# Kernel tuning notes

Measured on AMD Instinct MI355X. Metric: run time of the kernel, lower is better.

## Reference

```python
import jax, jax.numpy as jnp
import numpy as np

N_NODES = 100000
N_EDGES = 600000
N_GRAPHS = 8
D_IN = 256
H = 128
N_CONV = 2  # layers [128,128,128] -> first_h + 2 GINConvs
BN_EPS = 1e-5


def _bn_eval(x, p):
    # p: [4, H] rows = (gamma, beta, running_mean, running_var); eval-mode BatchNorm1d
    g, b, m, v = p[0], p[1], p[2], p[3]
    return (x - m) * jax.lax.rsqrt(v + BN_EPS) * g + b


def setup_inputs() -> dict:
    key = jax.random.key(0)
    ks = jax.random.split(key, 12)
    x = jax.random.normal(ks[0], (N_NODES, D_IN), dtype=jnp.float32)
    edge_index = jax.random.randint(ks[1], (2, N_EDGES), 0, N_NODES, dtype=jnp.int64 if jax.config.jax_enable_x64 else jnp.int32)
    batch = jnp.sort(jax.random.randint(ks[2], (N_NODES,), 0, N_GRAPHS))
    s = 0.05
    w_first = jax.random.normal(ks[3], (D_IN, H), dtype=jnp.float32) * s
    b_first = jax.random.normal(ks[4], (H,), dtype=jnp.float32) * s

    def bn_params(k):
        k1, k2, k3, k4 = jax.random.split(k, 4)
        gamma = jax.random.uniform(k1, (H,), minval=0.5, maxval=1.5)
        beta = jax.random.normal(k2, (H,)) * 0.1
        mean = jax.random.normal(k3, (H,)) * 0.1
        var = jax.random.uniform(k4, (H,), minval=0.5, maxval=1.5)
        return jnp.stack([gamma, beta, mean, var])  # [4, H]

    bn_first = bn_params(ks[5])
    w_conv = jax.random.normal(ks[6], (N_CONV, H, H), dtype=jnp.float32) * s
    b_conv = jax.random.normal(ks[7], (N_CONV, H), dtype=jnp.float32) * s
    bn_conv = jnp.stack([bn_params(k) for k in jax.random.split(ks[8], N_CONV)])  # [2,4,H]
    w_lin = jax.random.normal(ks[9], (N_CONV + 1, H, 1), dtype=jnp.float32) * s
    b_lin = jax.random.normal(ks[10], (N_CONV + 1, 1), dtype=jnp.float32) * s
    return {"x": x, "edge_index": edge_index, "batch": batch,
            "w_first": w_first, "b_first": b_first, "bn_first": bn_first,
            "w_conv": w_conv, "b_conv": b_conv, "bn_conv": bn_conv,
            "w_lin": w_lin, "b_lin": b_lin}


def reference(x, edge_index, batch, w_first, b_first, bn_first, w_conv, b_conv, bn_conv, w_lin, b_lin):
    src, dst = edge_index[0], edge_index[1]
    # first_h: Linear + BN(eval) + ReLU
    h = jax.nn.relu(_bn_eval(x @ w_first + b_first, bn_first))  # [N, H]

    # layer 0: node-level linear head + global max pool
    node_pred = h @ w_lin[0] + b_lin[0]  # [N, 1]
    wsi_pred = jax.ops.segment_max(node_pred, batch, num_segments=N_GRAPHS)  # [G, 1]

    for l in range(N_CONV):
        # GINConv (eps=0, sum aggregation): nn((1+eps)*x_i + sum_{j->i} x_j)
        agg = jax.ops.segment_sum(h[src], dst, num_segments=N_NODES)  # [N, H]
        h = jax.nn.relu(_bn_eval((h + agg) @ w_conv[l] + b_conv[l], bn_conv[l]))
        np_sub = h @ w_lin[l + 1] + b_lin[l + 1]  # [N, 1]
        node_pred = node_pred + np_sub
        wsi_pred = wsi_pred + jax.ops.segment_max(np_sub, batch, num_segments=N_GRAPHS)
        # dropout p=0.0 -> identity
    return wsi_pred, node_pred
```

## Files before the change

### kernel.cpp

```cpp
#include <hip/hip_runtime.h>
#include <hip/hip_bf16.h>

#define H 128
#define D_IN 256
#define NGRAPH 8

typedef __attribute__((ext_vector_type(8))) short bf16x8;
typedef __attribute__((ext_vector_type(4))) float f32x4;
typedef __attribute__((ext_vector_type(4))) int i32x4;

__device__ __forceinline__ unsigned fenc(float f) {
  unsigned u = __float_as_uint(f);
  return (u & 0x80000000u) ? ~u : (u | 0x80000000u);
}
__device__ __forceinline__ float fdec(unsigned e) {
  unsigned v = (e & 0x80000000u) ? (e & 0x7FFFFFFFu) : ~e;
  return __uint_as_float(v);
}
__device__ __forceinline__ unsigned short f2bf(float f) {
  unsigned u = __float_as_uint(f);
  unsigned r = u + 0x7FFFu + ((u >> 16) & 1u);
  return (unsigned short)(r >> 16);
}

__device__ __forceinline__ void gload16(const void* gsrc, void* ldst) {
  __builtin_amdgcn_global_load_lds(
      (const __attribute__((address_space(1))) unsigned int*)gsrc,
      (__attribute__((address_space(3))) unsigned int*)ldst, 16, 0, 0);
}

__global__ void init_kernel(int* __restrict__ offsets, int n1) {
  int i = blockIdx.x * blockDim.x + threadIdx.x;
  if (i < n1) offsets[i] = 0;
}

__global__ void count_kernel(const int* __restrict__ dst, int* __restrict__ offsets, int E) {
  int i = blockIdx.x * blockDim.x + threadIdx.x;
  int stride = gridDim.x * blockDim.x;
  for (int e = i; e < E; e += stride) atomicAdd(&offsets[dst[e]], 1);
}

__global__ void __launch_bounds__(1024)
scan_local(int* __restrict__ data, int* __restrict__ bsum, int n) {
  __shared__ int s[1024];
  int tid = threadIdx.x;
  int i = blockIdx.x * 1024 + tid;
  int v = (i < n) ? data[i] : 0;
  s[tid] = v;
  __syncthreads();
  for (int off = 1; off < 1024; off <<= 1) {
    int t = (tid >= off) ? s[tid - off] : 0;
    __syncthreads();
    s[tid] += t;
    __syncthreads();
  }
  if (i < n) data[i] = s[tid] - v;
  if (tid == 1023) bsum[blockIdx.x] = s[1023];
}

__global__ void __launch_bounds__(128)
scan_bsum(int* __restrict__ bsum, int nb) {
  __shared__ int s[128];
  int tid = threadIdx.x;
  int v = (tid < nb) ? bsum[tid] : 0;
  s[tid] = v;
  __syncthreads();
  for (int off = 1; off < 128; off <<= 1) {
    int t = (tid >= off) ? s[tid - off] : 0;
    __syncthreads();
    s[tid] += t;
    __syncthreads();
  }
  if (tid < nb) bsum[tid] = s[tid] - v;
}

__global__ void __launch_bounds__(1024)
scan_add(int* __restrict__ data, const int* __restrict__ bsum, int* __restrict__ cursor,
         int n, int ncur) {
  int i = blockIdx.x * 1024 + threadIdx.x;
  if (i < n) {
    int v = data[i] + bsum[blockIdx.x];
    data[i] = v;
    if (i < ncur) cursor[i] = v;
  }
}

__global__ void fill_kernel(const int* __restrict__ src, const int* __restrict__ dst,
                            int* __restrict__ cursor, int* __restrict__ esrc, int E) {
  int i = blockIdx.x * blockDim.x + threadIdx.x;
  int stride = gridDim.x * blockDim.x;
  for (int e = i; e < E; e += stride) {
    int d = dst[e];
    int p = atomicAdd(&cursor[d], 1);
    esrc[p] = src[e];
  }
}

__global__ void prep_weights(const float* __restrict__ wf, const float* __restrict__ wcv,
                             unsigned short* __restrict__ Bf, unsigned short* __restrict__ Bc) {
  int i = blockIdx.x * 256 + threadIdx.x;
  if (i < 32768) {
    int s = i >> 12, r = i & 4095;
    int c = r >> 5, r2 = r & 31;
    int g = r2 >> 3, j = r2 & 7;
    int k = s * 32 + g * 8 + j;
    Bf[i] = f2bf(wf[k * H + c]);
  } else {
    int i2 = i - 32768;
    int l = i2 >> 14, r = i2 & 16383;
    int s = r >> 12, rr = r & 4095;
    int c = rr >> 5, r2 = rr & 31;
    int g = r2 >> 3, j = r2 & 7;
    int k = s * 32 + g * 8 + j;
    Bc[i2] = f2bf(wcv[l * H * H + k * H + c]);
  }
}

template <int K, bool AF32, bool FIRST>
__global__ void __launch_bounds__(256, 4)
gemm_kernel(const void* __restrict__ Ain, const unsigned short* __restrict__ Bpack,
            const float* __restrict__ bias, const float* __restrict__ bn,
            const float* __restrict__ wlin, const float* __restrict__ blin, int lidx,
            const int* __restrict__ batch, unsigned short* __restrict__ hout,
            float* __restrict__ node_pred, unsigned* __restrict__ slot, int N) {
  constexpr int RB = 256;
  constexpr int ROWBYTES = AF32 ? K * 4 : K * 2;
  constexpr int NCHUNK = ROWBYTES / RB;
  constexpr int SPC = AF32 ? 2 : 4;
  __shared__ char s_a[64 * RB];
  __shared__ float s_head[64][2];
  __shared__ unsigned s_wsi[NGRAPH];
  const int tid = threadIdx.x;
  const int wid = tid >> 6, lane = tid & 63;
  const int wr = wid >> 1, wc = wid & 1;
  const int g = lane >> 4, l15 = lane & 15;
  const int row0blk = blockIdx.x * 64;
  if (tid < NGRAPH) s_wsi[tid] = 0u;

  f32x4 acc[2][4] = {};
  const int lrow0 = wr * 32;
  const char* Ab = (const char*)Ain;

  for (int ch = 0; ch < NCHUNK; ++ch) {
#pragma unroll
    for (int it = 0; it < 4; ++it) {
      int unit = it * 256 + tid;
      int lr = unit >> 4;
      int cb = (unit & 15) * 16;
      int grow = row0blk + lr;
      grow = (grow < N) ? grow : (N - 1);
      int gcol = cb ^ ((lr & 7) << 4);
      gload16(Ab + (size_t)grow * ROWBYTES + ch * RB + gcol,
              s_a + (it * 256 + wid * 64) * 16);
    }
    __syncthreads();

#pragma unroll
    for (int s = 0; s < SPC; ++s) {
      int sg = ch * SPC + s;
      bf16x8 bfr[4];
#pragma unroll
      for (int n = 0; n < 4; ++n) {
        int c = wc * 64 + n * 16 + l15;
        bfr[n] = *(const bf16x8*)(Bpack + sg * 4096 + c * 32 + g * 8);
      }
      bf16x8 af[2];
#pragma unroll
      for (int m = 0; m < 2; ++m) {
        int lr = lrow0 + m * 16 + l15;
        int sw = (lr & 7) << 4;
        if (AF32) {
          int c0 = s * 128 + g * 32;
          f32x4 u0 = *(const f32x4*)(s_a + lr * RB + (c0 ^ sw));
          f32x4 u1 = *(const f32x4*)(s_a + lr * RB + ((c0 + 16) ^ sw));
          union { unsigned short hh[8]; bf16x8 v; } pk;
          pk.hh[0] = f2bf(u0[0]); pk.hh[1] = f2bf(u0[1]);
          pk.hh[2] = f2bf(u0[2]); pk.hh[3] = f2bf(u0[3]);
          pk.hh[4] = f2bf(u1[0]); pk.hh[5] = f2bf(u1[1]);
          pk.hh[6] = f2bf(u1[2]); pk.hh[7] = f2bf(u1[3]);
          af[m] = pk.v;
        } else {
          int c0 = s * 64 + g * 16;
          af[m] = *(const bf16x8*)(s_a + lr * RB + (c0 ^ sw));
        }
      }
#pragma unroll
      for (int m = 0; m < 2; ++m)
#pragma unroll
        for (int n = 0; n < 4; ++n)
          acc[m][n] = __builtin_amdgcn_mfma_f32_16x16x32_bf16(af[m], bfr[n], acc[m][n], 0, 0, 0);
    }
    __syncthreads();
  }

  float sc[4], sh[4], wl[4];
#pragma unroll
  for (int n = 0; n < 4; ++n) {
    int c = wc * 64 + n * 16 + l15;
    float gam = bn[c], bet = bn[H + c], mu = bn[2 * H + c], va = bn[3 * H + c];
    float rs = rsqrtf(va + 1e-5f);
    sc[n] = gam * rs;
    sh[n] = (bias[c] - mu) * gam * rs + bet;
    wl[n] = wlin[c];
  }

  char* aw = s_a + wid * 2048;
#pragma unroll
  for (int m = 0; m < 2; ++m) {
    float pj[4] = {0.f, 0.f, 0.f, 0.f};
#pragma unroll
    for (int n = 0; n < 4; ++n)
#pragma unroll
      for (int j = 0; j < 4; ++j) {
        float hv = fmaxf(acc[m][n][j] * sc[n] + sh[n], 0.f);
        pj[j] += hv * wl[n];
        *(unsigned short*)(aw + (g * 4 + j) * 128 + (n * 16 + l15) * 2) = f2bf(hv);
      }
#pragma unroll
    for (int j = 0; j < 4; ++j) {
      pj[j] += __shfl_xor(pj[j], 1);
      pj[j] += __shfl_xor(pj[j], 2);
      pj[j] += __shfl_xor(pj[j], 4);
      pj[j] += __shfl_xor(pj[j], 8);
    }
    if (l15 == 0) {
#pragma unroll
      for (int j = 0; j < 4; ++j)
        s_head[wr * 32 + m * 16 + g * 4 + j][wc] = pj[j];
    }
    int grb = row0blk + wr * 32 + m * 16;
#pragma unroll
    for (int it = 0; it < 2; ++it) {
      int bo = lane * 16 + it * 1024;
      int r16 = bo >> 7, inrow = bo & 127;
      if (grb + r16 < N)
        *(i32x4*)((char*)hout + (size_t)(grb + r16) * 256 + wc * 128 + inrow) =
            *(i32x4*)(aw + bo);
    }
  }
  __syncthreads();
  if (tid < 64) {
    int grh = row0blk + tid;
    if (grh < N) {
      float np = s_head[tid][0] + s_head[tid][1] + blin[lidx];
      if (FIRST) node_pred[grh] = np; else node_pred[grh] += np;
      atomicMax(&s_wsi[batch[grh]], fenc(np));
    }
  }
  __syncthreads();
  if (tid < NGRAPH) slot[blockIdx.x * NGRAPH + tid] = s_wsi[tid];
}

__global__ void __launch_bounds__(256)
agg_kernel(const unsigned short* __restrict__ h, const int* __restrict__ offsets,
           const int* __restrict__ esrc, unsigned short* __restrict__ tmp, int n) {
  int node = blockIdx.x * 4 + (threadIdx.x >> 6);
  if (node >= n) return;
  int lane = threadIdx.x & 63;
  const unsigned* hw = (const unsigned*)h;
  size_t base = (size_t)node * (H / 2) + lane;
  unsigned u = hw[base];
  float a0 = __uint_as_float((u & 0xFFFFu) << 16);
  float a1 = __uint_as_float(u & 0xFFFF0000u);
  int s = offsets[node], e = offsets[node + 1];
  int j = s;
  for (; j + 4 <= e; j += 4) {
    int i0 = esrc[j], i1 = esrc[j + 1], i2 = esrc[j + 2], i3 = esrc[j + 3];
    unsigned v0 = hw[(size_t)i0 * (H / 2) + lane];
    unsigned v1 = hw[(size_t)i1 * (H / 2) + lane];
    unsigned v2 = hw[(size_t)i2 * (H / 2) + lane];
    unsigned v3 = hw[(size_t)i3 * (H / 2) + lane];
    a0 += __uint_as_float((v0 & 0xFFFFu) << 16) + __uint_as_float((v1 & 0xFFFFu) << 16) +
          __uint_as_float((v2 & 0xFFFFu) << 16) + __uint_as_float((v3 & 0xFFFFu) << 16);
    a1 += __uint_as_float(v0 & 0xFFFF0000u) + __uint_as_float(v1 & 0xFFFF0000u) +
          __uint_as_float(v2 & 0xFFFF0000u) + __uint_as_float(v3 & 0xFFFF0000u);
  }
  for (; j < e; ++j) {
    unsigned v2 = hw[(size_t)esrc[j] * (H / 2) + lane];
    a0 += __uint_as_float((v2 & 0xFFFFu) << 16);
    a1 += __uint_as_float(v2 & 0xFFFF0000u);
  }
  unsigned r = ((unsigned)f2bf(a1) << 16) | (unsigned)f2bf(a0);
  ((unsigned*)tmp)[base] = r;
}

__global__ void __launch_bounds__(256)
finalize_kernel(const unsigned* __restrict__ slots, float* __restrict__ out, int nb) {
  __shared__ float red[3][NGRAPH];
  int tid = threadIdx.x;
  if (tid < 192) {
    int pair = tid >> 3, w = tid & 7;
    int l = pair >> 3, g = pair & 7;
    unsigned m = 0u;
    const unsigned* base = slots + (size_t)l * nb * NGRAPH + g;
    for (int b = w; b < nb; b += 8) m = max(m, base[b * NGRAPH]);
    m = max(m, (unsigned)__shfl_xor((int)m, 1));
    m = max(m, (unsigned)__shfl_xor((int)m, 2));
    m = max(m, (unsigned)__shfl_xor((int)m, 4));
    if (w == 0) red[l][g] = fdec(m);
  }
  __syncthreads();
  if (tid < NGRAPH) out[tid] = red[0][tid] + red[1][tid] + red[2][tid];
}

extern "C" void kernel_launch(void* const* d_in, const int* in_sizes, int n_in,
                              void* d_out, int out_size, void* d_ws, size_t ws_size,
                              hipStream_t stream) {
  const float* x        = (const float*)d_in[0];
  const int*   ei       = (const int*)d_in[1];
  const int*   batch    = (const int*)d_in[2];
  const float* w_first  = (const float*)d_in[3];
  const float* b_first  = (const float*)d_in[4];
  const float* bn_first = (const float*)d_in[5];
  const float* w_conv   = (const float*)d_in[6];
  const float* b_conv   = (const float*)d_in[7];
  const float* bn_conv  = (const float*)d_in[8];
  const float* w_lin    = (const float*)d_in[9];
  const float* b_lin    = (const float*)d_in[10];
  float* out = (float*)d_out;

  const int N = in_sizes[0] / D_IN;
  const int E = in_sizes[1] / 2;
  const int* src = ei;
  const int* dst = ei + E;

  const int gemm_grid = (N + 63) / 64;

  char* ws = (char*)d_ws;
  unsigned short* h   = (unsigned short*)ws;
  unsigned short* tmp = h + (size_t)N * H;
  unsigned short* wTf = tmp + (size_t)N * H;
  unsigned short* wTc = wTf + H * D_IN;
  int* offsets = (int*)(wTc + 2 * H * H);
  int* cursor  = offsets + (N + 1);
  int* esrc    = cursor + N;
  int* bsum    = esrc + E;
  unsigned* slots = (unsigned*)(bsum + 128);
  float* node_pred = out + NGRAPH;

  const int nscan = N + 1;
  const int nb = (nscan + 1023) / 1024;

  init_kernel<<<(N + 256) / 256, 256, 0, stream>>>(offsets, N + 1);
  count_kernel<<<1024, 256, 0, stream>>>(dst, offsets, E);
  scan_local<<<nb, 1024, 0, stream>>>(offsets, bsum, nscan);
  scan_bsum<<<1, 128, 0, stream>>>(bsum, nb);
  scan_add<<<nb, 1024, 0, stream>>>(offsets, bsum, cursor, nscan, N);
  fill_kernel<<<1024, 256, 0, stream>>>(src, dst, cursor, esrc, E);
  prep_weights<<<256, 256, 0, stream>>>(w_first, w_conv, wTf, wTc);

  gemm_kernel<D_IN, true, true><<<gemm_grid, 256, 0, stream>>>(
      x, wTf, b_first, bn_first, w_lin, b_lin, 0, batch, h, node_pred, slots, N);
  for (int l = 0; l < 2; ++l) {
    agg_kernel<<<(N + 3) / 4, 256, 0, stream>>>(h, offsets, esrc, tmp, N);
    gemm_kernel<H, false, false><<<gemm_grid, 256, 0, stream>>>(
        tmp, wTc + (size_t)l * 16384, b_conv + (size_t)l * H, bn_conv + (size_t)l * 4 * H,
        w_lin + (size_t)(l + 1) * H, b_lin, l + 1, batch, h, node_pred,
        slots + (size_t)(l + 1) * gemm_grid * NGRAPH, N);
  }
  finalize_kernel<<<1, 256, 0, stream>>>(slots, out, gemm_grid);
}
```

Before: 253.1 us.

## Fuse whole pipeline into one cooperative persistent kernel with grid syncs

Replaces the chain of about a dozen kernel launches with a single cooperative mega-kernel, capped at 768 blocks, that uses grid.sync between the CSR build, weight packing, GEMM and aggregation phases. Per-block max-pool slots and the finalize reduction are replaced by global atomicMax into a small per-layer array. The aim is to remove launch gaps and inter-kernel drain overhead. In exchange, GEMM and aggregation now run persistent loops over tiles at lower occupancy, and each grid barrier has its own cost. A multi-kernel fallback path is kept in case the cooperative launch fails.

```diff
diff --git a/kernel.cpp b/kernel.cpp
--- a/kernel.cpp
+++ b/kernel.cpp
@@ -1,5 +1,8 @@
 #include <hip/hip_runtime.h>
 #include <hip/hip_bf16.h>
+#include <hip/hip_cooperative_groups.h>
+
+namespace cg = cooperative_groups;
 
 #define H 128
 #define D_IN 256
@@ -22,119 +25,30 @@
   unsigned r = u + 0x7FFFu + ((u >> 16) & 1u);
   return (unsigned short)(r >> 16);
 }
-
 __device__ __forceinline__ void gload16(const void* gsrc, void* ldst) {
   __builtin_amdgcn_global_load_lds(
       (const __attribute__((address_space(1))) unsigned int*)gsrc,
       (__attribute__((address_space(3))) unsigned int*)ldst, 16, 0, 0);
 }
 
-__global__ void init_kernel(int* __restrict__ offsets, int n1) {
-  int i = blockIdx.x * blockDim.x + threadIdx.x;
-  if (i < n1) offsets[i] = 0;
-}
-
-__global__ void count_kernel(const int* __restrict__ dst, int* __restrict__ offsets, int E) {
-  int i = blockIdx.x * blockDim.x + threadIdx.x;
-  int stride = gridDim.x * blockDim.x;
-  for (int e = i; e < E; e += stride) atomicAdd(&offsets[dst[e]], 1);
-}
-
-__global__ void __launch_bounds__(1024)
-scan_local(int* __restrict__ data, int* __restrict__ bsum, int n) {
-  __shared__ int s[1024];
-  int tid = threadIdx.x;
-  int i = blockIdx.x * 1024 + tid;
-  int v = (i < n) ? data[i] : 0;
-  s[tid] = v;
-  __syncthreads();
-  for (int off = 1; off < 1024; off <<= 1) {
-    int t = (tid >= off) ? s[tid - off] : 0;
-    __syncthreads();
-    s[tid] += t;
-    __syncthreads();
-  }
-  if (i < n) data[i] = s[tid] - v;
-  if (tid == 1023) bsum[blockIdx.x] = s[1023];
-}
-
-__global__ void __launch_bounds__(128)
-scan_bsum(int* __restrict__ bsum, int nb) {
-  __shared__ int s[128];
-  int tid = threadIdx.x;
-  int v = (tid < nb) ? bsum[tid] : 0;
-  s[tid] = v;
-  __syncthreads();
-  for (int off = 1; off < 128; off <<= 1) {
-    int t = (tid >= off) ? s[tid - off] : 0;
-    __syncthreads();
-    s[tid] += t;
-    __syncthreads();
-  }
-  if (tid < nb) bsum[tid] = s[tid] - v;
-}
-
-__global__ void __launch_bounds__(1024)
-scan_add(int* __restrict__ data, const int* __restrict__ bsum, int* __restrict__ cursor,
-         int n, int ncur) {
-  int i = blockIdx.x * 1024 + threadIdx.x;
-  if (i < n) {
-    int v = data[i] + bsum[blockIdx.x];
-    data[i] = v;
-    if (i < ncur) cursor[i] = v;
-  }
-}
-
-__global__ void fill_kernel(const int* __restrict__ src, const int* __restrict__ dst,
-                            int* __restrict__ cursor, int* __restrict__ esrc, int E) {
-  int i = blockIdx.x * blockDim.x + threadIdx.x;
-  int stride = gridDim.x * blockDim.x;
-  for (int e = i; e < E; e += stride) {
-    int d = dst[e];
-    int p = atomicAdd(&cursor[d], 1);
-    esrc[p] = src[e];
-  }
-}
-
-__global__ void prep_weights(const float* __restrict__ wf, const float* __restrict__ wcv,
-                             unsigned short* __restrict__ Bf, unsigned short* __restrict__ Bc) {
-  int i = blockIdx.x * 256 + threadIdx.x;
-  if (i < 32768) {
-    int s = i >> 12, r = i & 4095;
-    int c = r >> 5, r2 = r & 31;
-    int g = r2 >> 3, j = r2 & 7;
-    int k = s * 32 + g * 8 + j;
-    Bf[i] = f2bf(wf[k * H + c]);
-  } else {
-    int i2 = i - 32768;
-    int l = i2 >> 14, r = i2 & 16383;
-    int s = r >> 12, rr = r & 4095;
-    int c = rr >> 5, r2 = rr & 31;
-    int g = r2 >> 3, j = r2 & 7;
-    int k = s * 32 + g * 8 + j;
-    Bc[i2] = f2bf(wcv[l * H * H + k * H + c]);
-  }
-}
 
 template <int K, bool AF32, bool FIRST>
-__global__ void __launch_bounds__(256, 4)
-gemm_kernel(const void* __restrict__ Ain, const unsigned short* __restrict__ Bpack,
-            const float* __restrict__ bias, const float* __restrict__ bn,
-            const float* __restrict__ wlin, const float* __restrict__ blin, int lidx,
-            const int* __restrict__ batch, unsigned short* __restrict__ hout,
-            float* __restrict__ node_pred, unsigned* __restrict__ slot, int N) {
+__device__ void gemm_tile(int tile, const void* Ain, const unsigned short* Bpack,
+                          const float* bias, const float* bn, const float* wlin,
+                          float blinv, const int* batch, unsigned short* hout,
+                          float* node_pred, unsigned* wsiL, int N,
+                          char* s_a, float (*s_head)[2], unsigned* s_wsi) {
   constexpr int RB = 256;
   constexpr int ROWBYTES = AF32 ? K * 4 : K * 2;
   constexpr int NCHUNK = ROWBYTES / RB;
   constexpr int SPC = AF32 ? 2 : 4;
-  __shared__ char s_a[64 * RB];
-  __shared__ float s_head[64][2];
-  __shared__ unsigned s_wsi[NGRAPH];
   const int tid = threadIdx.x;
   const int wid = tid >> 6, lane = tid & 63;
   const int wr = wid >> 1, wc = wid & 1;
   const int g = lane >> 4, l15 = lane & 15;
-  const int row0blk = blockIdx.x * 64;
+  const int row0blk = tile * 64;
+
+  __syncthreads();
   if (tid < NGRAPH) s_wsi[tid] = 0u;
 
   f32x4 acc[2][4] = {};
@@ -242,121 +156,364 @@
   if (tid < 64) {
     int grh = row0blk + tid;
     if (grh < N) {
-      float np = s_head[tid][0] + s_head[tid][1] + blin[lidx];
+      float np = s_head[tid][0] + s_head[tid][1] + blinv;
       if (FIRST) node_pred[grh] = np; else node_pred[grh] += np;
       atomicMax(&s_wsi[batch[grh]], fenc(np));
     }
   }
   __syncthreads();
-  if (tid < NGRAPH) slot[blockIdx.x * NGRAPH + tid] = s_wsi[tid];
+  if (tid < NGRAPH && s_wsi[tid] != 0u) atomicMax(&wsiL[tid], s_wsi[tid]);
+}
+
+__device__ void agg_body(const unsigned short* h, const int* offsets, const int* esrc,
+                         unsigned short* tmp, int N) {
+  const int tid = threadIdx.x;
+  const int wid = tid >> 6, lane = tid & 63;
+  const int stride = gridDim.x * 4;
+  const unsigned* hw = (const unsigned*)h;
+  for (int node = blockIdx.x * 4 + wid; node < N; node += stride) {
+    size_t base = (size_t)node * 64 + lane;
+    unsigned u = hw[base];
+    float a0 = __uint_as_float((u & 0xFFFFu) << 16);
+    float a1 = __uint_as_float(u & 0xFFFF0000u);
+    int s = offsets[node], e = offsets[node + 1];
+    int j = s;
+    for (; j + 4 <= e; j += 4) {
+      int i0 = esrc[j], i1 = esrc[j + 1], i2 = esrc[j + 2], i3 = esrc[j + 3];
+      unsigned v0 = hw[(size_t)i0 * 64 + lane];
+      unsigned v1 = hw[(size_t)i1 * 64 + lane];
+      unsigned v2 = hw[(size_t)i2 * 64 + lane];
+      unsigned v3 = hw[(size_t)i3 * 64 + lane];
+      a0 += __uint_as_float((v0 & 0xFFFFu) << 16) + __uint_as_float((v1 & 0xFFFFu) << 16) +
+            __uint_as_float((v2 & 0xFFFFu) << 16) + __uint_as_float((v3 & 0xFFFFu) << 16);
+      a1 += __uint_as_float(v0 & 0xFFFF0000u) + __uint_as_float(v1 & 0xFFFF0000u) +
+            __uint_as_float(v2 & 0xFFFF0000u) + __uint_as_float(v3 & 0xFFFF0000u);
+    }
+    for (; j < e; ++j) {
+      unsigned v = hw[(size_t)esrc[j] * 64 + lane];
+      a0 += __uint_as_float((v & 0xFFFFu) << 16);
+      a1 += __uint_as_float(v & 0xFFFF0000u);
+    }
+    ((unsigned*)tmp)[base] = ((unsigned)f2bf(a1) << 16) | (unsigned)f2bf(a0);
+  }
+}
+
+__device__ void pack_weights_body(int i, const float* wf, const float* wcv,
+                                  unsigned short* Bf, unsigned short* Bc) {
+  if (i < 32768) {
+    int s = i >> 12, r = i & 4095;
+    int c = r >> 5, r2 = r & 31;
+    int g = r2 >> 3, j = r2 & 7;
+    int k = s * 32 + g * 8 + j;
+    Bf[i] = f2bf(wf[k * H + c]);
+  } else if (i < 65536) {
+    int i2 = i - 32768;
+    int l = i2 >> 14, r = i2 & 16383;
+    int s = r >> 12, rr = r & 4095;
+    int c = rr >> 5, r2 = rr & 31;
+    int g = r2 >> 3, j = r2 & 7;
+    int k = s * 32 + g * 8 + j;
+    Bc[i2] = f2bf(wcv[l * H * H + k * H + c]);
+  }
+}
+
+
+struct KArgs {
+  const float* x;
+  const int* src;
+  const int* dst;
+  const int* batch;
+  const float* w_first;
+  const float* b_first;
+  const float* bn_first;
+  const float* w_conv;
+  const float* b_conv;
+  const float* bn_conv;
+  const float* w_lin;
+  const float* b_lin;
+  float* out;
+  unsigned short* h;
+  unsigned short* tmp;
+  unsigned short* wTf;
+  unsigned short* wTc;
+  int* offsets;
+  int* cursor;
+  int* esrc;
+  int* csum;
+  unsigned* wsi;
+  int N, E, ntiles, nchunks;
+};
+
+__global__ void __launch_bounds__(256)
+mega_kernel(KArgs a) {
+  cg::grid_group grid = cg::this_grid();
+  __shared__ char s_a[16384];
+  __shared__ float s_head[64][2];
+  __shared__ unsigned s_wsi[NGRAPH];
+  int* s_scan = (int*)s_a;
+  int* s_c2 = (int*)(s_a + 1024);
+
+  const int tid = threadIdx.x;
+  const int bid = blockIdx.x;
+  const int gtid = bid * 256 + tid;
+  const int gstride = gridDim.x * 256;
+  const int n1 = a.N + 1;
+
+  for (int i = gtid; i < n1; i += gstride) a.offsets[i] = 0;
+  if (gtid < 3 * NGRAPH) a.wsi[gtid] = 0u;
+  for (int i = gtid; i < 65536; i += gstride)
+    pack_weights_body(i, a.w_first, a.w_conv, a.wTf, a.wTc);
+  grid.sync();
+
+  for (int e = gtid; e < a.E; e += gstride) atomicAdd(&a.offsets[a.dst[e]], 1);
+  grid.sync();
+
+  for (int ch = bid; ch < a.nchunks; ch += gridDim.x) {
+    int i = ch * 256 + tid;
+    int v = (i < n1) ? a.offsets[i] : 0;
+    s_scan[tid] = v;
+    __syncthreads();
+    for (int off = 1; off < 256; off <<= 1) {
+      int t = (tid >= off) ? s_scan[tid - off] : 0;
+      __syncthreads();
+      s_scan[tid] += t;
+      __syncthreads();
+    }
+    if (i < n1) a.offsets[i] = s_scan[tid] - v;
+    if (tid == 255) a.csum[ch] = s_scan[255];
+    __syncthreads();
+  }
+  grid.sync();
+
+  if (bid == 0) {
+    for (int k = tid; k < 512; k += 256) s_c2[k] = (k < a.nchunks) ? a.csum[k] : 0;
+    __syncthreads();
+    for (int off = 1; off < 512; off <<= 1) {
+      int t0 = (tid >= off) ? s_c2[tid - off] : 0;
+      int t1 = ((tid + 256) >= off) ? s_c2[tid + 256 - off] : 0;
+      __syncthreads();
+      s_c2[tid] += t0;
+      s_c2[tid + 256] += t1;
+      __syncthreads();
+    }
+    for (int k = tid; k < a.nchunks; k += 256) a.csum[k] = (k == 0) ? 0 : s_c2[k - 1];
+  }
+  grid.sync();
+
+  for (int i = gtid; i < n1; i += gstride) {
+    int v = a.offsets[i] + a.csum[i >> 8];
+    a.offsets[i] = v;
+    if (i < a.N) a.cursor[i] = v;
+  }
+  grid.sync();
+
+  for (int e = gtid; e < a.E; e += gstride) {
+    int d = a.dst[e];
+    int p = atomicAdd(&a.cursor[d], 1);
+    a.esrc[p] = a.src[e];
+  }
+  grid.sync();
+
+  float* node_pred = a.out + NGRAPH;
+
+  for (int t = bid; t < a.ntiles; t += gridDim.x)
+    gemm_tile<D_IN, true, true>(t, a.x, a.wTf, a.b_first, a.bn_first, a.w_lin,
+                                a.b_lin[0], a.batch, a.h, node_pred, a.wsi, a.N,
+                                s_a, s_head, s_wsi);
+  grid.sync();
+
+  agg_body(a.h, a.offsets, a.esrc, a.tmp, a.N);
+  grid.sync();
+
+  for (int t = bid; t < a.ntiles; t += gridDim.x)
+    gemm_tile<H, false, false>(t, a.tmp, a.wTc, a.b_conv, a.bn_conv, a.w_lin + H,
+                               a.b_lin[1], a.batch, a.h, node_pred, a.wsi + NGRAPH, a.N,
+                               s_a, s_head, s_wsi);
+  grid.sync();
+
+  agg_body(a.h, a.offsets, a.esrc, a.tmp, a.N);
+  grid.sync();
+
+  for (int t = bid; t < a.ntiles; t += gridDim.x)
+    gemm_tile<H, false, false>(t, a.tmp, a.wTc + 16384, a.b_conv + H, a.bn_conv + 4 * H,
+                               a.w_lin + 2 * H, a.b_lin[2], a.batch, a.h, node_pred,
+                               a.wsi + 2 * NGRAPH, a.N, s_a, s_head, s_wsi);
+  grid.sync();
+
+  if (bid == 0 && tid < NGRAPH)
+    a.out[tid] = fdec(a.wsi[tid]) + fdec(a.wsi[NGRAPH + tid]) + fdec(a.wsi[2 * NGRAPH + tid]);
+}
+
+
+__global__ void init_prep_kernel(int* __restrict__ offsets, int n1, unsigned* __restrict__ wsi,
+                                 const float* __restrict__ wf, const float* __restrict__ wcv,
+                                 unsigned short* __restrict__ Bf, unsigned short* __restrict__ Bc) {
+  int i = blockIdx.x * 256 + threadIdx.x;
+  if (i < n1) offsets[i] = 0;
+  if (i < 3 * NGRAPH) wsi[i] = 0u;
+  pack_weights_body(i, wf, wcv, Bf, Bc);
+}
+
+__global__ void count_kernel(const int* __restrict__ dst, int* __restrict__ offsets, int E) {
+  int i = blockIdx.x * blockDim.x + threadIdx.x;
+  int stride = gridDim.x * blockDim.x;
+  for (int e = i; e < E; e += stride) atomicAdd(&offsets[dst[e]], 1);
+}
+
+__global__ void __launch_bounds__(1024)
+scan_local(int* __restrict__ data, int* __restrict__ bsum, int n) {
+  __shared__ int s[1024];
+  int tid = threadIdx.x;
+  int i = blockIdx.x * 1024 + tid;
+  int v = (i < n) ? data[i] : 0;
+  s[tid] = v;
+  __syncthreads();
+  for (int off = 1; off < 1024; off <<= 1) {
+    int t = (tid >= off) ? s[tid - off] : 0;
+    __syncthreads();
+    s[tid] += t;
+    __syncthreads();
+  }
+  if (i < n) data[i] = s[tid] - v;
+  if (tid == 1023) bsum[blockIdx.x] = s[1023];
+}
+
+__global__ void __launch_bounds__(1024)
+scan_add2(int* __restrict__ data, const int* __restrict__ bsum, int* __restrict__ cursor,
+          int n, int ncur, int nb) {
+  __shared__ int sb[128];
+  int tid = threadIdx.x;
+  if (tid < 128) sb[tid] = (tid < nb) ? bsum[tid] : 0;
+  __syncthreads();
+  for (int off = 1; off < 128; off <<= 1) {
+    int t = (tid < 128 && tid >= off) ? sb[tid - off] : 0;
+    __syncthreads();
+    if (tid < 128) sb[tid] += t;
+    __syncthreads();
+  }
+  int add = (blockIdx.x == 0) ? 0 : sb[blockIdx.x - 1];
+  int i = blockIdx.x * 1024 + tid;
+  if (i < n) {
+    int v = data[i] + add;
+    data[i] = v;
+    if (i < ncur) cursor[i] = v;
+  }
+}
+
+__global__ void fill_kernel(const int* __restrict__ src, const int* __restrict__ dst,
+                            int* __restrict__ cursor, int* __restrict__ esrc, int E) {
+  int i = blockIdx.x * blockDim.x + threadIdx.x;
+  int stride = gridDim.x * blockDim.x;
+  for (int e = i; e < E; e += stride) {
+    int d = dst[e];
+    int p = atomicAdd(&cursor[d], 1);
+    esrc[p] = src[e];
+  }
+}
+
+template <int K, bool AF32, bool FIRST>
+__global__ void __launch_bounds__(256, 4)
+gemm_kernel(const void* __restrict__ Ain, const unsigned short* __restrict__ Bpack,
+            const float* __restrict__ bias, const float* __restrict__ bn,
+            const float* __restrict__ wlin, const float* __restrict__ blin, int lidx,
+            const int* __restrict__ batch, unsigned short* __restrict__ hout,
+            float* __restrict__ node_pred, unsigned* __restrict__ wsi, int N) {
+  __shared__ char s_a[16384];
+  __shared__ float s_head[64][2];
+  __shared__ unsigned s_wsi[NGRAPH];
+  gemm_tile<K, AF32, FIRST>(blockIdx.x, Ain, Bpack, bias, bn, wlin, blin[lidx], batch,
+                            hout, node_pred, wsi, N, s_a, s_head, s_wsi);
 }
 
 __global__ void __launch_bounds__(256)
 agg_kernel(const unsigned short* __restrict__ h, const int* __restrict__ offsets,
-           const int* __restrict__ esrc, unsigned short* __restrict__ tmp, int n) {
-  int node = blockIdx.x * 4 + (threadIdx.x >> 6);
-  if (node >= n) return;
-  int lane = threadIdx.x & 63;
-  const unsigned* hw = (const unsigned*)h;
-  size_t base = (size_t)node * (H / 2) + lane;
-  unsigned u = hw[base];
-  float a0 = __uint_as_float((u & 0xFFFFu) << 16);
-  float a1 = __uint_as_float(u & 0xFFFF0000u);
-  int s = offsets[node], e = offsets[node + 1];
-  int j = s;
-  for (; j + 4 <= e; j += 4) {
-    int i0 = esrc[j], i1 = esrc[j + 1], i2 = esrc[j + 2], i3 = esrc[j + 3];
-    unsigned v0 = hw[(size_t)i0 * (H / 2) + lane];
-    unsigned v1 = hw[(size_t)i1 * (H / 2) + lane];
-    unsigned v2 = hw[(size_t)i2 * (H / 2) + lane];
-    unsigned v3 = hw[(size_t)i3 * (H / 2) + lane];
-    a0 += __uint_as_float((v0 & 0xFFFFu) << 16) + __uint_as_float((v1 & 0xFFFFu) << 16) +
-          __uint_as_float((v2 & 0xFFFFu) << 16) + __uint_as_float((v3 & 0xFFFFu) << 16);
-    a1 += __uint_as_float(v0 & 0xFFFF0000u) + __uint_as_float(v1 & 0xFFFF0000u) +
-          __uint_as_float(v2 & 0xFFFF0000u) + __uint_as_float(v3 & 0xFFFF0000u);
-  }
-  for (; j < e; ++j) {
-    unsigned v2 = hw[(size_t)esrc[j] * (H / 2) + lane];
-    a0 += __uint_as_float((v2 & 0xFFFFu) << 16);
-    a1 += __uint_as_float(v2 & 0xFFFF0000u);
-  }
-  unsigned r = ((unsigned)f2bf(a1) << 16) | (unsigned)f2bf(a0);
-  ((unsigned*)tmp)[base] = r;
-}
-
-__global__ void __launch_bounds__(256)
-finalize_kernel(const unsigned* __restrict__ slots, float* __restrict__ out, int nb) {
-  __shared__ float red[3][NGRAPH];
-  int tid = threadIdx.x;
-  if (tid < 192) {
-    int pair = tid >> 3, w = tid & 7;
-    int l = pair >> 3, g = pair & 7;
-    unsigned m = 0u;
-    const unsigned* base = slots + (size_t)l * nb * NGRAPH + g;
-    for (int b = w; b < nb; b += 8) m = max(m, base[b * NGRAPH]);
-    m = max(m, (unsigned)__shfl_xor((int)m, 1));
-    m = max(m, (unsigned)__shfl_xor((int)m, 2));
-    m = max(m, (unsigned)__shfl_xor((int)m, 4));
-    if (w == 0) red[l][g] = fdec(m);
-  }
-  __syncthreads();
-  if (tid < NGRAPH) out[tid] = red[0][tid] + red[1][tid] + red[2][tid];
-}
+           const int* __restrict__ esrc, unsigned short* __restrict__ tmp, int N) {
+  agg_body(h, offsets, esrc, tmp, N);
+}
+
+__global__ void finalize_small(const unsigned* __restrict__ wsi, float* __restrict__ out) {
+  int g = threadIdx.x;
+  if (g < NGRAPH) out[g] = fdec(wsi[g]) + fdec(wsi[NGRAPH + g]) + fdec(wsi[2 * NGRAPH + g]);
+}
+
 
 extern "C" void kernel_launch(void* const* d_in, const int* in_sizes, int n_in,
                               void* d_out, int out_size, void* d_ws, size_t ws_size,
                               hipStream_t stream) {
-  const float* x        = (const float*)d_in[0];
-  const int*   ei       = (const int*)d_in[1];
-  const int*   batch    = (const int*)d_in[2];
-  const float* w_first  = (const float*)d_in[3];
-  const float* b_first  = (const float*)d_in[4];
-  const float* bn_first = (const float*)d_in[5];
-  const float* w_conv   = (const float*)d_in[6];
-  const float* b_conv   = (const float*)d_in[7];
-  const float* bn_conv  = (const float*)d_in[8];
-  const float* w_lin    = (const float*)d_in[9];
-  const float* b_lin    = (const float*)d_in[10];
-  float* out = (float*)d_out;
-
-  const int N = in_sizes[0] / D_IN;
-  const int E = in_sizes[1] / 2;
-  const int* src = ei;
-  const int* dst = ei + E;
-
-  const int gemm_grid = (N + 63) / 64;
+  KArgs a;
+  a.x        = (const float*)d_in[0];
+  const int* ei = (const int*)d_in[1];
+  a.batch    = (const int*)d_in[2];
+  a.w_first  = (const float*)d_in[3];
+  a.b_first  = (const float*)d_in[4];
+  a.bn_first = (const float*)d_in[5];
+  a.w_conv   = (const float*)d_in[6];
+  a.b_conv   = (const float*)d_in[7];
+  a.bn_conv  = (const float*)d_in[8];
+  a.w_lin    = (const float*)d_in[9];
+  a.b_lin    = (const float*)d_in[10];
+  a.out = (float*)d_out;
+
+  a.N = in_sizes[0] / D_IN;
+  a.E = in_sizes[1] / 2;
+  a.src = ei;
+  a.dst = ei + a.E;
+  a.ntiles = (a.N + 63) / 64;
+  a.nchunks = (a.N + 1 + 255) / 256;
 
   char* ws = (char*)d_ws;
-  unsigned short* h   = (unsigned short*)ws;
-  unsigned short* tmp = h + (size_t)N * H;
-  unsigned short* wTf = tmp + (size_t)N * H;
-  unsigned short* wTc = wTf + H * D_IN;
-  int* offsets = (int*)(wTc + 2 * H * H);
-  int* cursor  = offsets + (N + 1);
-  int* esrc    = cursor + N;
-  int* bsum    = esrc + E;
-  unsigned* slots = (unsigned*)(bsum + 128);
-  float* node_pred = out + NGRAPH;
-
-  const int nscan = N + 1;
-  const int nb = (nscan + 1023) / 1024;
-
-  init_kernel<<<(N + 256) / 256, 256, 0, stream>>>(offsets, N + 1);
-  count_kernel<<<1024, 256, 0, stream>>>(dst, offsets, E);
-  scan_local<<<nb, 1024, 0, stream>>>(offsets, bsum, nscan);
-  scan_bsum<<<1, 128, 0, stream>>>(bsum, nb);
-  scan_add<<<nb, 1024, 0, stream>>>(offsets, bsum, cursor, nscan, N);
-  fill_kernel<<<1024, 256, 0, stream>>>(src, dst, cursor, esrc, E);
-  prep_weights<<<256, 256, 0, stream>>>(w_first, w_conv, wTf, wTc);
-
-  gemm_kernel<D_IN, true, true><<<gemm_grid, 256, 0, stream>>>(
-      x, wTf, b_first, bn_first, w_lin, b_lin, 0, batch, h, node_pred, slots, N);
-  for (int l = 0; l < 2; ++l) {
-    agg_kernel<<<(N + 3) / 4, 256, 0, stream>>>(h, offsets, esrc, tmp, N);
+  a.h   = (unsigned short*)ws;
+  a.tmp = a.h + (size_t)a.N * H;
+  a.wTf = a.tmp + (size_t)a.N * H;
+  a.wTc = a.wTf + H * D_IN;
+  a.offsets = (int*)(a.wTc + 2 * H * H);
+  a.cursor  = a.offsets + (a.N + 1);
+  a.esrc    = a.cursor + a.N;
+  a.csum    = a.esrc + a.E;
+  a.wsi     = (unsigned*)(a.csum + 512);
+
+  hipError_t lerr = hipErrorUnknown;
+  int maxB = 0;
+  if (hipOccupancyMaxActiveBlocksPerMultiprocessor(&maxB, mega_kernel, 256, 0) == hipSuccess &&
+      maxB > 0) {
+    int dev = 0, nCU = 0;
+    hipGetDevice(&dev);
+    if (hipDeviceGetAttribute(&nCU, hipDeviceAttributeMultiprocessorCount, dev) != hipSuccess ||
+        nCU <= 0)
+      nCU = 256;
+    long long cap = (long long)maxB * nCU;
+    int grid = (cap > 768) ? 768 : (int)cap;
+    if (grid >= 64) {
+      void* kp[] = {(void*)&a};
+      lerr = hipLaunchCooperativeKernel(mega_kernel, dim3(grid), dim3(256), kp, 0, stream);
+    }
+  }
+
+  if (lerr != hipSuccess) {
+    const int N = a.N, E = a.E;
+    const int gemm_grid = a.ntiles;
+    const int nscan = N + 1;
+    const int nb = (nscan + 1023) / 1024;
+    float* node_pred = a.out + NGRAPH;
+
+    init_prep_kernel<<<(N + 256) / 256, 256, 0, stream>>>(a.offsets, nscan, a.wsi,
+                                                          a.w_first, a.w_conv, a.wTf, a.wTc);
+    count_kernel<<<1024, 256, 0, stream>>>(a.dst, a.offsets, E);
+    scan_local<<<nb, 1024, 0, stream>>>(a.offsets, a.csum, nscan);
+    scan_add2<<<nb, 1024, 0, stream>>>(a.offsets, a.csum, a.cursor, nscan, N, nb);
+    fill_kernel<<<1024, 256, 0, stream>>>(a.src, a.dst, a.cursor, a.esrc, E);
+
+    gemm_kernel<D_IN, true, true><<<gemm_grid, 256, 0, stream>>>(
+        a.x, a.wTf, a.b_first, a.bn_first, a.w_lin, a.b_lin, 0, a.batch, a.h,
+        node_pred, a.wsi, N);
+    agg_kernel<<<(N + 3) / 4, 256, 0, stream>>>(a.h, a.offsets, a.esrc, a.tmp, N);
     gemm_kernel<H, false, false><<<gemm_grid, 256, 0, stream>>>(
-        tmp, wTc + (size_t)l * 16384, b_conv + (size_t)l * H, bn_conv + (size_t)l * 4 * H,
-        w_lin + (size_t)(l + 1) * H, b_lin, l + 1, batch, h, node_pred,
-        slots + (size_t)(l + 1) * gemm_grid * NGRAPH, N);
-  }
-  finalize_kernel<<<1, 256, 0, stream>>>(slots, out, gemm_grid);
-}
+        a.tmp, a.wTc, a.b_conv, a.bn_conv, a.w_lin + H, a.b_lin, 1, a.batch, a.h,
+        node_pred, a.wsi + NGRAPH, N);
+    agg_kernel<<<(N + 3) / 4, 256, 0, stream>>>(a.h, a.offsets, a.esrc, a.tmp, N);
+    gemm_kernel<H, false, false><<<gemm_grid, 256, 0, stream>>>(
+        a.tmp, a.wTc + 16384, a.b_conv + H, a.bn_conv + 4 * H, a.w_lin + 2 * H, a.b_lin, 2,
+        a.batch, a.h, node_pred, a.wsi + 2 * NGRAPH, N);
+    finalize_small<<<1, 64, 0, stream>>>(a.wsi, a.out);
+  }
+}
```

Result: slower. 833.5 us (+229.3%).
